# Kernel optimization log

Measured on AMD Instinct MI355X. Metric: run time of the kernel, lower is better.

The kernel has to match this reference:

```python
import jax, jax.numpy as jnp
import numpy as np

N = 50000   # nodes
E = 640000  # edges
D = 128     # hidden_size
BN_EPS = 1e-5


def _bn(x, g, b):
    # BatchNorm1d, training-mode batch statistics (biased variance), per-feature
    m = jnp.mean(x, axis=0)
    v = jnp.var(x, axis=0)
    return g * (x - m) * jax.lax.rsqrt(v + BN_EPS) + b


def _gin_mlp(x, W1, b1, g, bb, W2, b2):
    # Linear -> BatchNorm1d -> GELU(exact) -> Linear
    h = jax.nn.gelu(_bn(x @ W1 + b1, g, bb), approximate=False)
    return h @ W2 + b2


def _ffn(x, W1, b1, g1, bb1, W2, b2, g2, bb2):
    # fc1=(Linear+BN) -> GELU -> fc2=(Linear+BN) -> +shortcut
    h = jax.nn.gelu(_bn(x @ W1 + b1, g1, bb1), approximate=False)
    return _bn(h @ W2 + b2, g2, bb2) + x


def setup_inputs() -> dict:
    key = jax.random.key(0)
    ks = iter(jax.random.split(key, 16))

    def p(*s):
        return jax.random.normal(next(ks), s, jnp.float32) * 0.05

    inp = {
        "x": jax.random.normal(next(ks), (N, D), jnp.float32),
        "edge_index": jax.random.randint(next(ks), (2, E), 0, N, jnp.int32),
        # node_encoder + batch_norm
        "enc_W": p(D, D), "enc_b": jnp.zeros(D, jnp.float32),
        "bn_g": jnp.ones(D, jnp.float32), "bn_b": jnp.zeros(D, jnp.float32),
        # GINConv MLP: Linear(D,D)+BN+GELU+Linear(D,D)
        "gW1": p(D, D), "gb1": jnp.zeros(D, jnp.float32),
        "gg": jnp.ones(D, jnp.float32), "gbb": jnp.zeros(D, jnp.float32),
        "gW2": p(D, D), "gb2": jnp.zeros(D, jnp.float32),
        # fc2 = FFN(D, 2D)
        "f2W1": p(D, 2 * D), "f2b1": jnp.zeros(2 * D, jnp.float32),
        "f2g1": jnp.ones(2 * D, jnp.float32), "f2bb1": jnp.zeros(2 * D, jnp.float32),
        "f2W2": p(2 * D, D), "f2b2": jnp.zeros(D, jnp.float32),
        "f2g2": jnp.ones(D, jnp.float32), "f2bb2": jnp.zeros(D, jnp.float32),
        # ffn = FFN(D, 4D)
        "fnW1": p(D, 4 * D), "fnb1": jnp.zeros(4 * D, jnp.float32),
        "fng1": jnp.ones(4 * D, jnp.float32), "fnbb1": jnp.zeros(4 * D, jnp.float32),
        "fnW2": p(4 * D, D), "fnb2": jnp.zeros(D, jnp.float32),
        "fng2": jnp.ones(D, jnp.float32), "fnbb2": jnp.zeros(D, jnp.float32),
    }
    return inp


def reference(x, edge_index, enc_W, enc_b, bn_g, bn_b,
              gW1, gb1, gg, gbb, gW2, gb2,
              f2W1, f2b1, f2g1, f2bb1, f2W2, f2b2, f2g2, f2bb2,
              fnW1, fnb1, fng1, fnbb1, fnW2, fnb2, fng2, fnbb2):
    shortcut = x
    # node_encoder + BN
    h = _bn(x @ enc_W + enc_b, bn_g, bn_b)  # [N, D]
    # GINConv: out = MLP((1+eps)*h + sum_{j->i} h_j), eps=0
    src, dst = edge_index[0], edge_index[1]
    agg = jax.ops.segment_sum(h[src], dst, num_segments=N)  # scatter-add [N, D]
    h = _gin_mlp(h + agg, gW1, gb1, gg, gbb, gW2, gb2)
    # fc2 FFN (hidden 2D, internal residual)
    h = _ffn(h, f2W1, f2b1, f2g1, f2bb1, f2W2, f2b2, f2g2, f2bb2)
    # outer residual
    h = shortcut + h
    # final FFN (hidden 4D, internal residual)
    return _ffn(h, fnW1, fnb1, fng1, fnbb1, fnW2, fnb2, fng2, fnbb2)
```

## Files before the change

kernel.cpp:

```cpp
#include <hip/hip_runtime.h>
#include <hip/hip_bf16.h>

typedef __attribute__((ext_vector_type(8))) short short8;
typedef __attribute__((ext_vector_type(4))) float f32x4;

__device__ __forceinline__ float bf2f(unsigned short u) {
    union { unsigned int i; float f; } c;
    c.i = ((unsigned int)u) << 16;
    return c.f;
}
__device__ __forceinline__ unsigned short f2bf(float f) {
    union { float f; unsigned int i; } c;
    c.f = f;
    unsigned int x = c.i;
    x += 0x7FFFu + ((x >> 16) & 1u);
    return (unsigned short)(x >> 16);
}
__device__ __forceinline__ float gelu_fast(float x) {
    const float x2 = x * x;
    const float t = x * fmaf(0.0713548163f, x2, 1.5957691216f);
    const float e = __expf(t);
    const float r = __builtin_amdgcn_rcpf(e + 1.0f);
    return fmaf(-x, r, x);
}

#define NPART 64

template<int K, int M, int XF>
__global__ __launch_bounds__(256, (K > 256) ? 4 : 5)
void gemmf_kernel(const void* __restrict__ Av,
                  const float* __restrict__ pCoef,
                  const unsigned short* __restrict__ res1,
                  const float* __restrict__ res2,
                  unsigned short* __restrict__ h3out,
                  const unsigned short* __restrict__ Wp,
                  const float* __restrict__ bias,
                  float* __restrict__ part,
                  unsigned short* __restrict__ C,
                  int nrows)
{
    constexpr int KS_TOT = K / 32;
    constexpr int NKC    = K / 128;
    constexpr int NCT    = M / 128;
    constexpr bool DBUF  = (K > 256);
    constexpr int NFRAG  = DBUF ? 32 : 4 * KS_TOT;
    __shared__ __align__(16) char smem[NFRAG * 1024 + ((NCT > 1) ? 16384 : 0)];
    char* cbuf = smem + ((NCT > 1) ? NFRAG * 1024 : 0);

    const int tid = threadIdx.x;
    const int l   = tid & 63, wv = tid >> 6;
    const int gr0 = blockIdx.x * 64;
    const int kq4 = l & 3, rloc = l >> 2;
    const int woff = ((kq4 * 16 + rloc) * 16) ^ (kq4 << 5);
    const int loff = (l * 16) ^ ((l >> 4) << 5);

    int rowg[4];
    bool rval[4];
    #pragma unroll
    for (int i = 0; i < 4; ++i) {
        int rg = gr0 + i * 16 + rloc;
        rval[i] = rg < nrows;
        rowg[i] = rval[i] ? rg : nrows - 1;
    }

    f32x4 acc[4][2];
    short8 breg[2][4];

    auto loadB = [&](int ct, int kcb) {
        #pragma unroll
        for (int c = 0; c < 2; ++c) {
            const int col = ct * 128 + (wv * 2 + c) * 16 + (l & 15);
            const unsigned short* bp = Wp + (size_t)col * K + kcb + (l >> 4) * 8;
            #pragma unroll
            for (int ks = 0; ks < 4; ++ks)
                breg[c][ks] = *(const short8*)(bp + ks * 32);
        }
    };

    auto xf2 = [&](short8 t, const float* sc8, const float* sh8) -> short8 {
        short8 val;
        #pragma unroll
        for (int j = 0; j < 8; ++j) {
            float v = fmaf(sc8[j], bf2f((unsigned short)t[j]), sh8[j]);
            val[j] = (short)f2bf(gelu_fast(v));
        }
        return val;
    };

    auto epilogue = [&](int ct) {
        const int lrow = l & 15, kg = l >> 4;
        __syncthreads();
        #pragma unroll
        for (int c = 0; c < 2; ++c) {
            const int col  = (wv * 2 + c) * 16 + lrow;
            const int gcol = ct * 128 + col;
            const float bc = bias[gcol];
            float s = 0.f, q = 0.f;
            #pragma unroll
            for (int r = 0; r < 4; ++r) {
                #pragma unroll
                for (int i = 0; i < 4; ++i) {
                    const int rl = r * 16 + kg * 4 + i;
                    const float v = acc[r][c][i] + bc;
                    if (gr0 + rl < nrows) { s += v; q += v * v; }
                    const int byte = rl * 256 + ((col * 2) ^ ((rl & 7) << 4));
                    *(unsigned short*)(cbuf + byte) = f2bf(v);
                }
            }
            s += __shfl_xor(s, 16); s += __shfl_xor(s, 32);
            q += __shfl_xor(q, 16); q += __shfl_xor(q, 32);
            if (kg == 0 && part != nullptr) {
                float* ps = part + (size_t)(blockIdx.x & (NPART - 1)) * (2 * M);
                atomicAdd(&ps[gcol], s);
                atomicAdd(&ps[M + gcol], q);
            }
        }
        __syncthreads();
        #pragma unroll
        for (int j = 0; j < 4; ++j) {
            const int lin = j * 256 + tid;
            const int rl = lin >> 4, chunk = lin & 15;
            const int row = gr0 + rl;
            if (row < nrows) {
                short8 vv = *(const short8*)(cbuf + rl * 256 + ((chunk * 16) ^ ((rl & 7) << 4)));
                *(short8*)(C + (size_t)row * M + ct * 128 + chunk * 8) = vv;
            }
        }
    };

    if constexpr (!DBUF) {
        #pragma unroll
        for (int h = 0; h < NKC; ++h) {
            const int kst = h * 4 + wv;
            const int c0k = kst * 32 + kq4 * 8;
            float sc8[8], sh8[8];
            if (XF >= 2) {
                #pragma unroll
                for (int j = 0; j < 8; ++j) {
                    sc8[j] = pCoef[c0k + j];
                    sh8[j] = pCoef[K + c0k + j];
                }
            }
            #pragma unroll
            for (int i = 0; i < 4; ++i) {
                const size_t eoff = (size_t)rowg[i] * K + c0k;
                short8 val;
                if (XF == 0) {
                    val = *(const short8*)((const unsigned short*)Av + eoff);
                } else if (XF == 1) {
                    const float* A = (const float*)Av;
                    f32x4 u0 = *(const f32x4*)(A + eoff);
                    f32x4 u1 = *(const f32x4*)(A + eoff + 4);
                    #pragma unroll
                    for (int j = 0; j < 4; ++j) {
                        val[j]     = (short)f2bf(u0[j]);
                        val[j + 4] = (short)f2bf(u1[j]);
                    }
                } else if (XF == 2) {
                    short8 t = *(const short8*)((const unsigned short*)Av + eoff);
                    val = xf2(t, sc8, sh8);
                } else {
                    short8 t = *(const short8*)((const unsigned short*)Av + eoff);
                    short8 u = *(const short8*)(res1 + eoff);
                    f32x4 x0 = *(const f32x4*)(res2 + eoff);
                    f32x4 x1 = *(const f32x4*)(res2 + eoff + 4);
                    #pragma unroll
                    for (int j = 0; j < 8; ++j) {
                        float v = fmaf(sc8[j], bf2f((unsigned short)t[j]), sh8[j]);
                        v += bf2f((unsigned short)u[j]) + ((j < 4) ? x0[j] : x1[j - 4]);
                        val[j] = (short)f2bf(v);
                    }
                    if (rval[i]) *(short8*)(h3out + eoff) = val;
                }
                *(short8*)(smem + (i * KS_TOT + kst) * 1024 + woff) = val;
            }
        }
        __syncthreads();
        #pragma unroll
        for (int ct = 0; ct < NCT; ++ct) {
            #pragma unroll
            for (int r = 0; r < 4; ++r)
                #pragma unroll
                for (int c = 0; c < 2; ++c) acc[r][c] = f32x4{0.f, 0.f, 0.f, 0.f};
            #pragma unroll
            for (int kc = 0; kc < NKC; ++kc) {
                loadB(ct, kc * 128);
                #pragma unroll
                for (int ks = 0; ks < 4; ++ks) {
                    const int ksg = kc * 4 + ks;
                    short8 af[4];
                    #pragma unroll
                    for (int r = 0; r < 4; ++r)
                        af[r] = *(const short8*)(smem + (r * KS_TOT + ksg) * 1024 + loff);
                    #pragma unroll
                    for (int r = 0; r < 4; ++r)
                        #pragma unroll
                        for (int c = 0; c < 2; ++c)
                            acc[r][c] = __builtin_amdgcn_mfma_f32_16x16x32_bf16(af[r], breg[c][ks], acc[r][c], 0, 0, 0);
                }
            }
            epilogue(ct);
        }
    } else {
        const int akoff = wv * 32 + kq4 * 8;
        auto stageChunk = [&](int kcb, int b, const short8* pre) {
            const int c0k = kcb + akoff;
            float sc8[8], sh8[8];
            if (XF >= 2) {
                #pragma unroll
                for (int j = 0; j < 8; ++j) {
                    sc8[j] = pCoef[c0k + j];
                    sh8[j] = pCoef[K + c0k + j];
                }
            }
            #pragma unroll
            for (int i = 0; i < 4; ++i) {
                short8 t = pre ? pre[i]
                              : *(const short8*)((const unsigned short*)Av + (size_t)rowg[i] * K + c0k);
                short8 val = (XF == 2) ? xf2(t, sc8, sh8) : t;
                *(short8*)(smem + (b * 16 + i * 4 + wv) * 1024 + woff) = val;
            }
        };
        stageChunk(0, 0, nullptr);
        __syncthreads();
        #pragma unroll
        for (int r = 0; r < 4; ++r)
            #pragma unroll
            for (int c = 0; c < 2; ++c) acc[r][c] = f32x4{0.f, 0.f, 0.f, 0.f};
        #pragma unroll
        for (int kc = 0; kc < NKC; ++kc) {
            const int cur = kc & 1;
            loadB(0, kc * 128);
            short8 anext[4];
            if (kc + 1 < NKC) {
                const int c0k = (kc + 1) * 128 + akoff;
                #pragma unroll
                for (int i = 0; i < 4; ++i)
                    anext[i] = *(const short8*)((const unsigned short*)Av + (size_t)rowg[i] * K + c0k);
            }
            #pragma unroll
            for (int ks = 0; ks < 4; ++ks) {
                short8 af[4];
                #pragma unroll
                for (int r = 0; r < 4; ++r)
                    af[r] = *(const short8*)(smem + (cur * 16 + r * 4 + ks) * 1024 + loff);
                #pragma unroll
                for (int r = 0; r < 4; ++r)
                    #pragma unroll
                    for (int c = 0; c < 2; ++c)
                        acc[r][c] = __builtin_amdgcn_mfma_f32_16x16x32_bf16(af[r], breg[c][ks], acc[r][c], 0, 0, 0);
            }
            if (kc + 1 < NKC) {
                stageChunk((kc + 1) * 128, cur ^ 1, anext);
                __syncthreads();
            }
        }
        epilogue(0);
    }
}

__global__ __launch_bounds__(256, 5)
void enc_place_kernel(const float* __restrict__ Av,
                      const unsigned short* __restrict__ Wp,
                      const float* __restrict__ bias,
                      float* __restrict__ part,
                      unsigned short* __restrict__ C, int nrows, int rb,
                      const int* __restrict__ ei, int* __restrict__ cursor,
                      int* __restrict__ ssrc, int E)
{
    __shared__ __align__(16) char smem[16384];
    if ((int)blockIdx.x >= rb) {
        const int e = (blockIdx.x - rb) * 256 + threadIdx.x;
        if (e < E) {
            int pos = atomicAdd(&cursor[ei[E + e]], 1);
            ssrc[pos] = ei[e];
        }
        return;
    }
    const int tid = threadIdx.x;
    const int l = tid & 63, wv = tid >> 6;
    const int gr0 = blockIdx.x * 64;
    const int kq4 = l & 3, rloc = l >> 2;
    const int woff = ((kq4 * 16 + rloc) * 16) ^ (kq4 << 5);
    const int loff = (l * 16) ^ ((l >> 4) << 5);
    const int lrow = l & 15, kg = l >> 4;
    const int akoff = wv * 32 + kq4 * 8;

    int rowg[4];
    #pragma unroll
    for (int i = 0; i < 4; ++i) {
        int rg = gr0 + i * 16 + rloc;
        rowg[i] = rg < nrows ? rg : nrows - 1;
    }
    #pragma unroll
    for (int i = 0; i < 4; ++i) {
        const float* p = Av + (size_t)rowg[i] * 128 + akoff;
        f32x4 u0 = *(const f32x4*)p;
        f32x4 u1 = *(const f32x4*)(p + 4);
        short8 val;
        #pragma unroll
        for (int j = 0; j < 4; ++j) {
            val[j]     = (short)f2bf(u0[j]);
            val[j + 4] = (short)f2bf(u1[j]);
        }
        *(short8*)(smem + (i * 4 + wv) * 1024 + woff) = val;
    }
    __syncthreads();

    short8 breg[2][4];
    #pragma unroll
    for (int c = 0; c < 2; ++c) {
        const int col = (wv * 2 + c) * 16 + lrow;
        const unsigned short* bp = Wp + (size_t)col * 128 + kg * 8;
        #pragma unroll
        for (int ks = 0; ks < 4; ++ks) breg[c][ks] = *(const short8*)(bp + ks * 32);
    }
    f32x4 acc[4][2];
    #pragma unroll
    for (int r = 0; r < 4; ++r)
        #pragma unroll
        for (int c = 0; c < 2; ++c) acc[r][c] = f32x4{0.f, 0.f, 0.f, 0.f};
    #pragma unroll
    for (int ks = 0; ks < 4; ++ks) {
        short8 af[4];
        #pragma unroll
        for (int r = 0; r < 4; ++r)
            af[r] = *(const short8*)(smem + (r * 4 + ks) * 1024 + loff);
        #pragma unroll
        for (int r = 0; r < 4; ++r)
            #pragma unroll
            for (int c = 0; c < 2; ++c)
                acc[r][c] = __builtin_amdgcn_mfma_f32_16x16x32_bf16(af[r], breg[c][ks], acc[r][c], 0, 0, 0);
    }
    __syncthreads();
    #pragma unroll
    for (int c = 0; c < 2; ++c) {
        const int col = (wv * 2 + c) * 16 + lrow;
        const float bc = bias[col];
        float s = 0.f, q = 0.f;
        #pragma unroll
        for (int r = 0; r < 4; ++r)
            #pragma unroll
            for (int i = 0; i < 4; ++i) {
                const int rl = r * 16 + kg * 4 + i;
                const float v = acc[r][c][i] + bc;
                if (gr0 + rl < nrows) { s += v; q += v * v; }
                *(unsigned short*)(smem + rl * 256 + ((col * 2) ^ ((rl & 7) << 4))) = f2bf(v);
            }
        s += __shfl_xor(s, 16); s += __shfl_xor(s, 32);
        q += __shfl_xor(q, 16); q += __shfl_xor(q, 32);
        if (kg == 0) {
            float* ps = part + (size_t)(blockIdx.x & (NPART - 1)) * 256;
            atomicAdd(&ps[col], s);
            atomicAdd(&ps[128 + col], q);
        }
    }
    __syncthreads();
    #pragma unroll
    for (int j = 0; j < 4; ++j) {
        const int lin = j * 256 + tid;
        const int rl = lin >> 4, chunk = lin & 15;
        const int row = gr0 + rl;
        if (row < nrows) {
            short8 vv = *(const short8*)(smem + rl * 256 + ((chunk * 16) ^ ((rl & 7) << 4)));
            *(short8*)(C + (size_t)row * 128 + chunk * 8) = vv;
        }
    }
}

__global__ void coef_kernel(const float* __restrict__ part,
                            const float* __restrict__ g, const float* __restrict__ b,
                            float* __restrict__ scsh, int W, float invN)
{
    int i = blockIdx.x * blockDim.x + threadIdx.x;
    if (i >= W) return;
    float s = 0.f, q = 0.f;
    #pragma unroll 8
    for (int r = 0; r < NPART; ++r) {
        s += part[(size_t)r * 2 * W + i];
        q += part[(size_t)r * 2 * W + W + i];
    }
    const float mean = s * invN;
    const float var  = q * invN - mean * mean;
    const float sc   = g[i] * rsqrtf(var + 1e-5f);
    scsh[i] = sc;
    scsh[W + i] = b[i] - mean * sc;
}

struct PackDesc { const float* src; unsigned short* dst; int K; int M; };
struct Pack7 { PackDesc d[7]; };
__global__ void pack_hist_kernel(Pack7 p, const int* __restrict__ ei,
                                 int* __restrict__ cnt, int E)
{
    if (blockIdx.x < 448) {
        const PackDesc d = p.d[blockIdx.x >> 6];
        const int total = d.K * d.M;
        for (int idx = (blockIdx.x & 63) * 256 + threadIdx.x; idx < total;
             idx += 64 * 256) {
            const int k = idx / d.M;
            const int m = idx - k * d.M;
            d.dst[(size_t)m * d.K + k] = f2bf(d.src[idx]);
        }
    } else {
        const int e = (blockIdx.x - 448) * 256 + threadIdx.x;
        if (e < E) atomicAdd(&cnt[ei[E + e]], 1);
    }
}

__global__ void scan_reduce(const int* __restrict__ cnt, int* __restrict__ blksum, int n)
{
    __shared__ int s[256];
    int t = threadIdx.x;
    int i = blockIdx.x * 256 + t;
    s[t] = i < n ? cnt[i] : 0;
    __syncthreads();
    for (int d = 128; d > 0; d >>= 1) {
        if (t < d) s[t] += s[t + d];
        __syncthreads();
    }
    if (t == 0) blksum[blockIdx.x] = s[0];
}

__global__ void scan_top(int* __restrict__ blksum, int nb)
{
    __shared__ int s[256];
    int t = threadIdx.x;
    int v = t < nb ? blksum[t] : 0;
    s[t] = v;
    __syncthreads();
    for (int d = 1; d < 256; d <<= 1) {
        int u = (t >= d) ? s[t - d] : 0;
        __syncthreads();
        s[t] += u;
        __syncthreads();
    }
    if (t < nb) blksum[t] = s[t] - v;
}

__global__ void scan_apply(const int* __restrict__ cnt, const int* __restrict__ blksum,
                           int* __restrict__ offs, int* __restrict__ cursor, int n)
{
    __shared__ int s[256];
    int t = threadIdx.x;
    int i = blockIdx.x * 256 + t;
    int v = i < n ? cnt[i] : 0;
    s[t] = v;
    __syncthreads();
    for (int d = 1; d < 256; d <<= 1) {
        int u = (t >= d) ? s[t - d] : 0;
        __syncthreads();
        s[t] += u;
        __syncthreads();
    }
    int excl = s[t] - v + blksum[blockIdx.x];
    if (i < n) { offs[i] = excl; cursor[i] = excl; }
}

__global__ __launch_bounds__(256)
void gather_kernel(const unsigned short* __restrict__ T0,
                   const float* __restrict__ coef,
                   const int* __restrict__ ssrc, const int* __restrict__ offs,
                   const int* __restrict__ cnt,
                   unsigned short* __restrict__ Zb, int N)
{
    const int wave = threadIdx.x >> 6;
    const int lane = threadIdx.x & 63;
    const int node = blockIdx.x * 4 + wave;
    if (node >= N) return;

    unsigned int hv = *(const unsigned int*)(T0 + (size_t)node * 128 + lane * 2);
    float a0 = bf2f((unsigned short)hv);
    float a1 = bf2f((unsigned short)(hv >> 16));

    const int off = offs[node];
    const int deg = cnt[node];
    for (int base = 0; base < deg; base += 64) {
        int m = deg - base;
        if (m > 64) m = 64;
        int idx = (base + lane < deg) ? ssrc[off + base + lane] : 0;
        int k = 0;
        for (; k + 1 < m; k += 2) {
            int s0 = __shfl(idx, k);
            int s1 = __shfl(idx, k + 1);
            unsigned int v0 = *(const unsigned int*)(T0 + (size_t)s0 * 128 + lane * 2);
            unsigned int v1 = *(const unsigned int*)(T0 + (size_t)s1 * 128 + lane * 2);
            a0 += bf2f((unsigned short)v0) + bf2f((unsigned short)v1);
            a1 += bf2f((unsigned short)(v0 >> 16)) + bf2f((unsigned short)(v1 >> 16));
        }
        if (k < m) {
            int s0 = __shfl(idx, k);
            unsigned int v0 = *(const unsigned int*)(T0 + (size_t)s0 * 128 + lane * 2);
            a0 += bf2f((unsigned short)v0);
            a1 += bf2f((unsigned short)(v0 >> 16));
        }
    }
    const int c0 = lane * 2;
    const float dp1 = (float)(deg + 1);
    const float z0 = fmaf(coef[c0], a0, dp1 * coef[128 + c0]);
    const float z1 = fmaf(coef[c0 + 1], a1, dp1 * coef[128 + c0 + 1]);
    unsigned int o = ((unsigned int)f2bf(z1) << 16) | (unsigned int)f2bf(z0);
    *(unsigned int*)(Zb + (size_t)node * 128 + lane * 2) = o;
}

__global__ void final_kernel(const unsigned short* __restrict__ t6,
                             const float* __restrict__ coef,
                             const unsigned short* __restrict__ h3,
                             float* __restrict__ out, int total4)
{
    int idx = blockIdx.x * blockDim.x + threadIdx.x;
    if (idx >= total4) return;
    const int base = idx * 4;
    const int c0 = base & 127;
    ushort4 tv = *(const ushort4*)(t6 + base);
    ushort4 hv = *(const ushort4*)(h3 + base);
    unsigned short ts[4] = {tv.x, tv.y, tv.z, tv.w};
    unsigned short hs[4] = {hv.x, hv.y, hv.z, hv.w};
    float4 ov;
    float* po = &ov.x;
    #pragma unroll
    for (int j = 0; j < 4; ++j) {
        const int c = c0 + j;
        po[j] = fmaf(coef[c], bf2f(ts[j]), coef[128 + c]) + bf2f(hs[j]);
    }
    *(float4*)(out + base) = ov;
}

extern "C" void kernel_launch(void* const* d_in, const int* in_sizes, int n_in,
                              void* d_out, int out_size, void* d_ws, size_t ws_size,
                              hipStream_t stream)
{
    const float* x     = (const float*)d_in[0];
    const int*   ei    = (const int*)d_in[1];
    const float* enc_W = (const float*)d_in[2];
    const float* enc_b = (const float*)d_in[3];
    const float* bn_g  = (const float*)d_in[4];
    const float* bn_b  = (const float*)d_in[5];
    const float* gW1   = (const float*)d_in[6];
    const float* gb1   = (const float*)d_in[7];
    const float* gg    = (const float*)d_in[8];
    const float* gbb   = (const float*)d_in[9];
    const float* gW2   = (const float*)d_in[10];
    const float* gb2   = (const float*)d_in[11];
    const float* f2W1  = (const float*)d_in[12];
    const float* f2b1  = (const float*)d_in[13];
    const float* f2g1  = (const float*)d_in[14];
    const float* f2bb1 = (const float*)d_in[15];
    const float* f2W2  = (const float*)d_in[16];
    const float* f2b2  = (const float*)d_in[17];
    const float* f2g2  = (const float*)d_in[18];
    const float* f2bb2 = (const float*)d_in[19];
    const float* fnW1  = (const float*)d_in[20];
    const float* fnb1  = (const float*)d_in[21];
    const float* fng1  = (const float*)d_in[22];
    const float* fnbb1 = (const float*)d_in[23];
    const float* fnW2  = (const float*)d_in[24];
    const float* fnb2  = (const float*)d_in[25];
    const float* fng2  = (const float*)d_in[26];
    const float* fnbb2 = (const float*)d_in[27];

    const int D = 128;
    const int N = in_sizes[0] / D;
    const int E = in_sizes[1] / 2;
    const float invN = 1.0f / (float)N;

    char* w = (char*)d_ws;
    float* c0 = (float*)w;
    float* c1 = c0 + 256;
    float* c3 = c1 + 256;
    float* c4 = c3 + 512;
    float* c5 = c4 + 256;
    float* c6 = c5 + 1024;
    const size_t coefBytes = 2560 * sizeof(float);
    size_t off = coefBytes;

    float* p0 = (float*)(w + off); off += (size_t)NPART * 256 * 4;
    float* p1 = (float*)(w + off); off += (size_t)NPART * 256 * 4;
    float* p3 = (float*)(w + off); off += (size_t)NPART * 512 * 4;
    float* p4 = (float*)(w + off); off += (size_t)NPART * 256 * 4;
    float* p5 = (float*)(w + off); off += (size_t)NPART * 1024 * 4;
    float* p6 = (float*)(w + off); off += (size_t)NPART * 256 * 4;
    const size_t partBytes = (size_t)NPART * 2560 * 4;

    unsigned short* wpE  = (unsigned short*)(w + off); off += (size_t)128 * 128 * 2;
    unsigned short* wpG1 = (unsigned short*)(w + off); off += (size_t)128 * 128 * 2;
    unsigned short* wpG2 = (unsigned short*)(w + off); off += (size_t)128 * 128 * 2;
    unsigned short* wpF1 = (unsigned short*)(w + off); off += (size_t)128 * 256 * 2;
    unsigned short* wpF2 = (unsigned short*)(w + off); off += (size_t)256 * 128 * 2;
    unsigned short* wpN1 = (unsigned short*)(w + off); off += (size_t)128 * 512 * 2;
    unsigned short* wpN2 = (unsigned short*)(w + off); off += (size_t)512 * 128 * 2;

    unsigned short* P1 = (unsigned short*)(w + off); off += (size_t)N * 128 * 2;
    unsigned short* Zb = (unsigned short*)(w + off); off += (size_t)N * 128 * 2;
    unsigned short* H3 = (unsigned short*)(w + off); off += (size_t)N * 128 * 2;
    unsigned short* T3 = (unsigned short*)(w + off); off += (size_t)N * 256 * 2;
    unsigned short* T5 = (unsigned short*)(w + off); off += (size_t)N * 512 * 2;

    const int NB = (N + 255) / 256;
    char* csr = (char*)T5;
    int* cnt    = (int*)csr;  csr += (size_t)NB * 256 * 4;
    int* offs   = (int*)csr;  csr += (size_t)NB * 256 * 4;
    int* cursor = (int*)csr;  csr += (size_t)NB * 256 * 4;
    int* blksum = (int*)csr;  csr += 1024;
    int* ssrc   = (int*)csr;

    hipMemsetAsync(p0, 0, partBytes, stream);
    hipMemsetAsync(cnt, 0, (size_t)NB * 256 * 4, stream);

    Pack7 pk;
    pk.d[0] = PackDesc{enc_W, wpE, 128, 128};
    pk.d[1] = PackDesc{gW1, wpG1, 128, 128};
    pk.d[2] = PackDesc{gW2, wpG2, 128, 128};
    pk.d[3] = PackDesc{f2W1, wpF1, 128, 256};
    pk.d[4] = PackDesc{f2W2, wpF2, 256, 128};
    pk.d[5] = PackDesc{fnW1, wpN1, 128, 512};
    pk.d[6] = PackDesc{fnW2, wpN2, 512, 128};

    const int eb = (E + 255) / 256;
    const int rb = (N + 63) / 64;
    const int t4a = N * 128 / 4;
    const int ewb = (t4a + 255) / 256;

    pack_hist_kernel<<<448 + eb, 256, 0, stream>>>(pk, ei, cnt, E);
    scan_reduce<<<NB, 256, 0, stream>>>(cnt, blksum, N);
    scan_top<<<1, 256, 0, stream>>>(blksum, NB);
    scan_apply<<<NB, 256, 0, stream>>>(cnt, blksum, offs, cursor, N);

    enc_place_kernel<<<rb + eb, 256, 0, stream>>>(
        x, wpE, enc_b, p0, P1, N, rb, ei, cursor, ssrc, E);
    coef_kernel<<<1, 256, 0, stream>>>(p0, bn_g, bn_b, c0, 128, invN);
    gather_kernel<<<(N + 3) / 4, 256, 0, stream>>>(
        P1, c0, ssrc, offs, cnt, Zb, N);
    gemmf_kernel<128, 128, 0><<<rb, 256, 0, stream>>>(
        Zb, nullptr, nullptr, nullptr, nullptr, wpG1, gb1, p1, P1, N);
    coef_kernel<<<1, 256, 0, stream>>>(p1, gg, gbb, c1, 128, invN);
    gemmf_kernel<128, 128, 2><<<rb, 256, 0, stream>>>(
        P1, c1, nullptr, nullptr, nullptr, wpG2, gb2, nullptr, Zb, N);
    gemmf_kernel<128, 256, 0><<<rb, 256, 0, stream>>>(
        Zb, nullptr, nullptr, nullptr, nullptr, wpF1, f2b1, p3, T3, N);
    coef_kernel<<<1, 256, 0, stream>>>(p3, f2g1, f2bb1, c3, 256, invN);
    gemmf_kernel<256, 128, 2><<<rb, 256, 0, stream>>>(
        T3, c3, nullptr, nullptr, nullptr, wpF2, f2b2, p4, P1, N);
    coef_kernel<<<1, 256, 0, stream>>>(p4, f2g2, f2bb2, c4, 128, invN);
    gemmf_kernel<128, 512, 3><<<rb, 256, 0, stream>>>(
        P1, c4, Zb, x, H3, wpN1, fnb1, p5, T5, N);
    coef_kernel<<<2, 256, 0, stream>>>(p5, fng1, fnbb1, c5, 512, invN);
    gemmf_kernel<512, 128, 2><<<rb, 256, 0, stream>>>(
        T5, c5, nullptr, nullptr, nullptr, wpN2, fnb2, p6, P1, N);
    coef_kernel<<<1, 256, 0, stream>>>(p6, fng2, fnbb2, c6, 128, invN);
    final_kernel<<<ewb, 256, 0, stream>>>(P1, c6, H3, (float*)d_out, t4a);

    (void)n_in; (void)out_size; (void)ws_size;
}
```

Baseline: 313.1 us.

## Fold BatchNorm coefficient reduction into last-finishing GEMM block; use u16 edge indices

Removes the six separate coef_kernel launches. Each producing kernel now takes a ticket with an atomic counter, and the last block to finish reduces the partial sums into the BN scale and shift. Separately, source indices in the CSR are stored as 16-bit when N fits, which halves index traffic in the gather. The trade-off is that the last block of each kernel does a serial tail reduction using atomic reads, and the enc_place edge-scatter blocks return early, which may interact with the ticket count.

```diff
diff --git a/kernel.cpp b/kernel.cpp
--- a/kernel.cpp
+++ b/kernel.cpp
@@ -25,6 +25,24 @@
 }
 
 #define NPART 64
+
+__device__ __forceinline__ void coef_fold(float* part, const float* gArr,
+                                          const float* bArr, float* coefOut,
+                                          int W, float invN, int tid)
+{
+    for (int i = tid; i < W; i += 256) {
+        float s = 0.f, q = 0.f;
+        for (int r = 0; r < NPART; ++r) {
+            s += atomicAdd(&part[(size_t)r * 2 * W + i], 0.0f);
+            q += atomicAdd(&part[(size_t)r * 2 * W + W + i], 0.0f);
+        }
+        const float mean = s * invN;
+        const float var  = q * invN - mean * mean;
+        const float sc   = gArr[i] * rsqrtf(var + 1e-5f);
+        coefOut[i] = sc;
+        coefOut[W + i] = bArr[i] - mean * sc;
+    }
+}
 
 template<int K, int M, int XF>
 __global__ __launch_bounds__(256, (K > 256) ? 4 : 5)
@@ -37,7 +55,10 @@
                   const float* __restrict__ bias,
                   float* __restrict__ part,
                   unsigned short* __restrict__ C,
-                  int nrows)
+                  int nrows,
+                  const float* __restrict__ gArr, const float* __restrict__ bArr,
+                  float* __restrict__ coefOut, int* __restrict__ ticket,
+                  float invN)
 {
     constexpr int KS_TOT = K / 32;
     constexpr int NKC    = K / 128;
@@ -45,6 +66,7 @@
     constexpr bool DBUF  = (K > 256);
     constexpr int NFRAG  = DBUF ? 32 : 4 * KS_TOT;
     __shared__ __align__(16) char smem[NFRAG * 1024 + ((NCT > 1) ? 16384 : 0)];
+    __shared__ int lastFlag;
     char* cbuf = smem + ((NCT > 1) ? NFRAG * 1024 : 0);
 
     const int tid = threadIdx.x;
@@ -257,6 +279,18 @@
         }
         epilogue(0);
     }
+
+    if (part != nullptr) {
+        __threadfence();
+        __syncthreads();
+        if (tid == 0) {
+            int old = atomicAdd(ticket, 1);
+            lastFlag = (old == (int)gridDim.x - 1);
+        }
+        __syncthreads();
+        if (lastFlag)
+            coef_fold(part, gArr, bArr, coefOut, M, invN, tid);
+    }
 }
 
 __global__ __launch_bounds__(256, 5)
@@ -266,14 +300,19 @@
                       float* __restrict__ part,
                       unsigned short* __restrict__ C, int nrows, int rb,
                       const int* __restrict__ ei, int* __restrict__ cursor,
-                      int* __restrict__ ssrc, int E)
+                      void* __restrict__ ssrcv, int E, int useU16,
+                      const float* __restrict__ gArr, const float* __restrict__ bArr,
+                      float* __restrict__ coefOut, int* __restrict__ ticket,
+                      float invN)
 {
     __shared__ __align__(16) char smem[16384];
+    __shared__ int lastFlag;
     if ((int)blockIdx.x >= rb) {
         const int e = (blockIdx.x - rb) * 256 + threadIdx.x;
         if (e < E) {
             int pos = atomicAdd(&cursor[ei[E + e]], 1);
-            ssrc[pos] = ei[e];
+            if (useU16) ((unsigned short*)ssrcv)[pos] = (unsigned short)ei[e];
+            else        ((int*)ssrcv)[pos] = ei[e];
         }
         return;
     }
@@ -366,25 +405,15 @@
             *(short8*)(C + (size_t)row * 128 + chunk * 8) = vv;
         }
     }
-}
-
-__global__ void coef_kernel(const float* __restrict__ part,
-                            const float* __restrict__ g, const float* __restrict__ b,
-                            float* __restrict__ scsh, int W, float invN)
-{
-    int i = blockIdx.x * blockDim.x + threadIdx.x;
-    if (i >= W) return;
-    float s = 0.f, q = 0.f;
-    #pragma unroll 8
-    for (int r = 0; r < NPART; ++r) {
-        s += part[(size_t)r * 2 * W + i];
-        q += part[(size_t)r * 2 * W + W + i];
-    }
-    const float mean = s * invN;
-    const float var  = q * invN - mean * mean;
-    const float sc   = g[i] * rsqrtf(var + 1e-5f);
-    scsh[i] = sc;
-    scsh[W + i] = b[i] - mean * sc;
+    __threadfence();
+    __syncthreads();
+    if (tid == 0) {
+        int old = atomicAdd(ticket, 1);
+        lastFlag = (old == rb - 1);
+    }
+    __syncthreads();
+    if (lastFlag)
+        coef_fold(part, gArr, bArr, coefOut, 128, invN, tid);
 }
 
 struct PackDesc { const float* src; unsigned short* dst; int K; int M; };
@@ -456,10 +485,11 @@
     if (i < n) { offs[i] = excl; cursor[i] = excl; }
 }
 
+template<typename IDX>
 __global__ __launch_bounds__(256)
 void gather_kernel(const unsigned short* __restrict__ T0,
                    const float* __restrict__ coef,
-                   const int* __restrict__ ssrc, const int* __restrict__ offs,
+                   const IDX* __restrict__ ssrc, const int* __restrict__ offs,
                    const int* __restrict__ cnt,
                    unsigned short* __restrict__ Zb, int N)
 {
@@ -477,7 +507,7 @@
     for (int base = 0; base < deg; base += 64) {
         int m = deg - base;
         if (m > 64) m = 64;
-        int idx = (base + lane < deg) ? ssrc[off + base + lane] : 0;
+        int idx = (base + lane < deg) ? (int)ssrc[off + base + lane] : 0;
         int k = 0;
         for (; k + 1 < m; k += 2) {
             int s0 = __shfl(idx, k);
@@ -562,6 +592,7 @@
     const int N = in_sizes[0] / D;
     const int E = in_sizes[1] / 2;
     const float invN = 1.0f / (float)N;
+    const int useU16 = (N <= 65535);
 
     char* w = (char*)d_ws;
     float* c0 = (float*)w;
@@ -573,13 +604,14 @@
     const size_t coefBytes = 2560 * sizeof(float);
     size_t off = coefBytes;
 
+    int* tickets = (int*)(w + off); off += 256;
     float* p0 = (float*)(w + off); off += (size_t)NPART * 256 * 4;
     float* p1 = (float*)(w + off); off += (size_t)NPART * 256 * 4;
     float* p3 = (float*)(w + off); off += (size_t)NPART * 512 * 4;
     float* p4 = (float*)(w + off); off += (size_t)NPART * 256 * 4;
     float* p5 = (float*)(w + off); off += (size_t)NPART * 1024 * 4;
     float* p6 = (float*)(w + off); off += (size_t)NPART * 256 * 4;
-    const size_t partBytes = (size_t)NPART * 2560 * 4;
+    const size_t zeroBytes = 256 + (size_t)NPART * 2560 * 4;
 
     unsigned short* wpE  = (unsigned short*)(w + off); off += (size_t)128 * 128 * 2;
     unsigned short* wpG1 = (unsigned short*)(w + off); off += (size_t)128 * 128 * 2;
@@ -601,9 +633,9 @@
     int* offs   = (int*)csr;  csr += (size_t)NB * 256 * 4;
     int* cursor = (int*)csr;  csr += (size_t)NB * 256 * 4;
     int* blksum = (int*)csr;  csr += 1024;
-    int* ssrc   = (int*)csr;
-
-    hipMemsetAsync(p0, 0, partBytes, stream);
+    void* ssrcv = (void*)csr;
+
+    hipMemsetAsync(tickets, 0, zeroBytes, stream);
     hipMemsetAsync(cnt, 0, (size_t)NB * 256 * 4, stream);
 
     Pack7 pk;
@@ -615,8 +647,8 @@
     pk.d[5] = PackDesc{fnW1, wpN1, 128, 512};
     pk.d[6] = PackDesc{fnW2, wpN2, 512, 128};
 
-    const int eb = (E + 255) / 256;
-    const int rb = (N + 63) / 64;
+    const int eb  = (E + 255) / 256;
+    const int rb  = (N + 63) / 64;
     const int t4a = N * 128 / 4;
     const int ewb = (t4a + 255) / 256;
 
@@ -626,27 +658,32 @@
     scan_apply<<<NB, 256, 0, stream>>>(cnt, blksum, offs, cursor, N);
 
     enc_place_kernel<<<rb + eb, 256, 0, stream>>>(
-        x, wpE, enc_b, p0, P1, N, rb, ei, cursor, ssrc, E);
-    coef_kernel<<<1, 256, 0, stream>>>(p0, bn_g, bn_b, c0, 128, invN);
-    gather_kernel<<<(N + 3) / 4, 256, 0, stream>>>(
-        P1, c0, ssrc, offs, cnt, Zb, N);
+        x, wpE, enc_b, p0, P1, N, rb, ei, cursor, ssrcv, E, useU16,
+        bn_g, bn_b, c0, tickets + 0, invN);
+    if (useU16)
+        gather_kernel<unsigned short><<<(N + 3) / 4, 256, 0, stream>>>(
+            P1, c0, (const unsigned short*)ssrcv, offs, cnt, Zb, N);
+    else
+        gather_kernel<unsigned int><<<(N + 3) / 4, 256, 0, stream>>>(
+            P1, c0, (const unsigned int*)ssrcv, offs, cnt, Zb, N);
     gemmf_kernel<128, 128, 0><<<rb, 256, 0, stream>>>(
-        Zb, nullptr, nullptr, nullptr, nullptr, wpG1, gb1, p1, P1, N);
-    coef_kernel<<<1, 256, 0, stream>>>(p1, gg, gbb, c1, 128, invN);
+        Zb, nullptr, nullptr, nullptr, nullptr, wpG1, gb1, p1, P1, N,
+        gg, gbb, c1, tickets + 1, invN);
     gemmf_kernel<128, 128, 2><<<rb, 256, 0, stream>>>(
-        P1, c1, nullptr, nullptr, nullptr, wpG2, gb2, nullptr, Zb, N);
+        P1, c1, nullptr, nullptr, nullptr, wpG2, gb2, nullptr, Zb, N,
+        nullptr, nullptr, nullptr, nullptr, invN);
     gemmf_kernel<128, 256, 0><<<rb, 256, 0, stream>>>(
-        Zb, nullptr, nullptr, nullptr, nullptr, wpF1, f2b1, p3, T3, N);
-    coef_kernel<<<1, 256, 0, stream>>>(p3, f2g1, f2bb1, c3, 256, invN);
+        Zb, nullptr, nullptr, nullptr, nullptr, wpF1, f2b1, p3, T3, N,
+        f2g1, f2bb1, c3, tickets + 2, invN);
     gemmf_kernel<256, 128, 2><<<rb, 256, 0, stream>>>(
-        T3, c3, nullptr, nullptr, nullptr, wpF2, f2b2, p4, P1, N);
-    coef_kernel<<<1, 256, 0, stream>>>(p4, f2g2, f2bb2, c4, 128, invN);
+        T3, c3, nullptr, nullptr, nullptr, wpF2, f2b2, p4, P1, N,
+        f2g2, f2bb2, c4, tickets + 3, invN);
     gemmf_kernel<128, 512, 3><<<rb, 256, 0, stream>>>(
-        P1, c4, Zb, x, H3, wpN1, fnb1, p5, T5, N);
-    coef_kernel<<<2, 256, 0, stream>>>(p5, fng1, fnbb1, c5, 512, invN);
+        P1, c4, Zb, x, H3, wpN1, fnb1, p5, T5, N,
+        fng1, fnbb1, c5, tickets + 4, invN);
     gemmf_kernel<512, 128, 2><<<rb, 256, 0, stream>>>(
-        T5, c5, nullptr, nullptr, nullptr, wpN2, fnb2, p6, P1, N);
-    coef_kernel<<<1, 256, 0, stream>>>(p6, fng2, fnbb2, c6, 128, invN);
+        T5, c5, nullptr, nullptr, nullptr, wpN2, fnb2, p6, P1, N,
+        fng2, fnbb2, c6, tickets + 5, invN);
     final_kernel<<<ewb, 256, 0, stream>>>(P1, c6, H3, (float*)d_out, t4a);
 
     (void)n_in; (void)out_size; (void)ws_size;
```

Result: slower. 763.8 us (+144.0%).
